# Performance work log

Measured on AMD Instinct MI355X. Metric: run time of the kernel, lower is better.

## Reference

```python
import jax, jax.numpy as jnp
import numpy as np

EPS = 1e-5

def layer_norm(x, g, b):
    mu = jnp.mean(x, axis=-1, keepdims=True)
    var = jnp.mean(jnp.square(x - mu), axis=-1, keepdims=True)
    return (x - mu) * jax.lax.rsqrt(var + EPS) * g + b

def setup_inputs() -> dict:
    key = jax.random.key(0)
    ks = jax.random.split(key, 8)
    B, N, C, H = 1, 384, 128, 128
    s = 0.02
    return {
        "pair": jax.random.normal(ks[0], (B, N, N, C), dtype=jnp.float32),
        "ln_l_g": jnp.ones((C,), jnp.float32), "ln_l_b": jnp.zeros((C,), jnp.float32),
        "ln_r_g": jnp.ones((C,), jnp.float32), "ln_r_b": jnp.zeros((C,), jnp.float32),
        "Wl": jax.random.normal(ks[1], (C, H), jnp.float32) * s, "bl": jnp.zeros((H,), jnp.float32),
        "Wr": jax.random.normal(ks[2], (C, H), jnp.float32) * s, "br": jnp.zeros((H,), jnp.float32),
        "Wg": jax.random.normal(ks[3], (C, H), jnp.float32) * s, "bg": jnp.zeros((H,), jnp.float32),
        "Wo": jax.random.normal(ks[4], (H, C), jnp.float32) * s, "bo": jnp.zeros((C,), jnp.float32),
        "n_g": jnp.ones((C,), jnp.float32), "n_b": jnp.zeros((C,), jnp.float32),
    }

def reference(pair, ln_l_g, ln_l_b, ln_r_g, ln_r_b, Wl, bl, Wr, br, Wg, bg, Wo, bo, n_g, n_b):
    # pair: [B, N, N, C]
    left = layer_norm(pair, ln_l_g, ln_l_b) @ Wl + bl      # [B,N,N,H]
    right = layer_norm(pair, ln_r_g, ln_r_b) @ Wr + br     # [B,N,N,H]
    gate = jax.nn.sigmoid(pair @ Wg + bg)                  # [B,N,N,H]
    # triangle multiplicative update: per-channel N x N matmul over k
    out = jnp.einsum('bikh,bkjh->bijh', left, right)
    out = out * gate
    out = out @ Wo + bo                                    # [B,N,N,C]
    return layer_norm(out + pair, n_g, n_b)
```

## Files before the change

### kernel.cpp

```cpp
#include <hip/hip_runtime.h>
#include <hip/hip_bf16.h>

#define N_ 384
#define C_ 128
#define M_ (N_*N_)

typedef __attribute__((ext_vector_type(8))) short bf16x8_t;
typedef __attribute__((ext_vector_type(4))) float f32x4_t;
typedef unsigned int u32;
typedef unsigned short u16;
typedef unsigned long long u64;

__device__ __forceinline__ u16 f2bf(float f) {
  u32 u = __builtin_bit_cast(u32, f);
  u32 r = (u + 0x7FFFu + ((u >> 16) & 1u)) >> 16;
  return (u16)r;
}
__device__ __forceinline__ float bf2f(u16 h) {
  u32 u = ((u32)h) << 16;
  return __builtin_bit_cast(float, u);
}

__global__ __launch_bounds__(256) void k_prep(const float* __restrict__ lg, const float* __restrict__ rg,
    const float* __restrict__ Wl, const float* __restrict__ Wr, const float* __restrict__ Wg,
    const float* __restrict__ Wo,
    const float* __restrict__ lb, const float* __restrict__ rb,
    const float* __restrict__ bl, const float* __restrict__ br, const float* __restrict__ bg,
    u16* __restrict__ wcat, u16* __restrict__ wot,
    float* __restrict__ bcat, float* __restrict__ sg) {
  int bx = blockIdx.x, t = threadIdx.x;
  if (bx < 256) {
    int idx = bx*256 + t;
    if (idx < 49152) {
      int n = idx >> 7, k = idx & 127;
      float v;
      if (n < 128)      v = lg[k] * Wl[k*128 + n];
      else if (n < 256) v = rg[k] * Wr[k*128 + (n-128)];
      else              v = Wg[k*128 + (n-256)];
      wcat[idx] = f2bf(v);
    } else {
      int i2 = idx - 49152;
      int c = i2 >> 7, h = i2 & 127;
      wot[i2] = f2bf(Wo[h*128 + c]);
    }
  } else if (bx == 256) {
    float s = 0.f;
    if (t < 128)      { for (int k=0;k<128;k++) s += lb[k]*Wl[k*128+t];       s += bl[t];     bcat[t] = s; }
    else              { int hh=t-128; for (int k=0;k<128;k++) s += rb[k]*Wr[k*128+hh]; s += br[hh]; bcat[t] = s; }
  } else {
    if (t < 128)      { bcat[256+t] = bg[t]; }
    else              { int hh = t-128; float s=0.f; for (int k=0;k<128;k++) s += Wg[k*128+hh]; sg[hh] = s; }
  }
}

#define LDK 136
#define LDA 72
#define LDW 72
#define LDT 136

__global__ __launch_bounds__(512) void k_projln(const float* __restrict__ pair,
    const u16* __restrict__ wcat, const float* __restrict__ bcat, const float* __restrict__ sg,
    u16* __restrict__ lr_, u16* __restrict__ gate_) {
  __shared__ u16 At[128*LDK];
  __shared__ float mu_s[128];
  __shared__ float irs_s[128];
  int bx = blockIdx.x;
  int r0 = bx * 128;
  int t = threadIdx.x, w = t>>6, lane = t&63;
  int q = lane>>4, nl = lane&15;

  {
    int rr = t >> 2, quarter = t & 3;
    const float4* gp = (const float4*)(pair + (size_t)(r0+rr)*128 + quarter*32);
    float4 v[8];
    #pragma unroll
    for (int i=0;i<8;i++) v[i] = gp[i];
    float s=0.f, qq=0.f;
    #pragma unroll
    for (int i=0;i<8;i++) {
      s  += v[i].x + v[i].y + v[i].z + v[i].w;
      qq += v[i].x*v[i].x + v[i].y*v[i].y + v[i].z*v[i].z + v[i].w*v[i].w;
    }
    s  += __shfl_xor(s, 1, 64);
    s  += __shfl_xor(s, 2, 64);
    qq += __shfl_xor(qq, 1, 64);
    qq += __shfl_xor(qq, 2, 64);
    float mu = s * (1.f/128.f);
    float var = qq*(1.f/128.f) - mu*mu;
    float rstd = rsqrtf(var + 1e-5f);
    if (quarter == 0) { mu_s[rr] = mu; irs_s[rr] = 1.0f/rstd; }
    u32* lp = (u32*)(At + rr*LDK + quarter*32);
    #pragma unroll
    for (int i=0;i<4;i++) {
      u32 p0 = (u32)f2bf((v[2*i].x-mu)*rstd)   | ((u32)f2bf((v[2*i].y-mu)*rstd)<<16);
      u32 p1 = (u32)f2bf((v[2*i].z-mu)*rstd)   | ((u32)f2bf((v[2*i].w-mu)*rstd)<<16);
      u32 p2 = (u32)f2bf((v[2*i+1].x-mu)*rstd) | ((u32)f2bf((v[2*i+1].y-mu)*rstd)<<16);
      u32 p3 = (u32)f2bf((v[2*i+1].z-mu)*rstd) | ((u32)f2bf((v[2*i+1].w-mu)*rstd)<<16);
      ((uint4*)lp)[i] = make_uint4(p0,p1,p2,p3);
    }
  }
  __syncthreads();

  #pragma unroll 1
  for (int nb = 0; nb < 3; ++nb) {
    const u16* bbase = wcat + (size_t)(nb*128)*128;
    f32x4_t acc[8] = {};
    #pragma unroll
    for (int ks=0; ks<4; ks++) {
      int kel = ks*32 + q*8;
      bf16x8_t b = *(const bf16x8_t*)(bbase + (size_t)(w*16 + nl)*128 + kel);
      #pragma unroll
      for (int tm=0;tm<8;tm++) {
        bf16x8_t a = *(const bf16x8_t*)(At + (tm*16+nl)*LDK + kel);
        acc[tm] = __builtin_amdgcn_mfma_f32_16x16x32_bf16(a, b, acc[tm], 0,0,0);
      }
    }
    int n = w*16 + nl;
    float bias = bcat[nb*128 + n];
    u16* rowp;
    if (nb == 0)      rowp = lr_   + ((size_t)bx*256 + n)*128;
    else if (nb == 1) rowp = lr_   + ((size_t)bx*256 + 128 + n)*128;
    else              rowp = gate_ + ((size_t)bx*128 + n)*128;
    if (nb == 2) {
      float sgn = sg[n];
      #pragma unroll
      for (int tm=0;tm<8;tm++) {
        f32x4_t mu4 = *(const f32x4_t*)(mu_s  + tm*16 + q*4);
        f32x4_t ir4 = *(const f32x4_t*)(irs_s + tm*16 + q*4);
        float v0 = acc[tm][0]*ir4[0] + mu4[0]*sgn + bias;
        float v1 = acc[tm][1]*ir4[1] + mu4[1]*sgn + bias;
        float v2 = acc[tm][2]*ir4[2] + mu4[2]*sgn + bias;
        float v3 = acc[tm][3]*ir4[3] + mu4[3]*sgn + bias;
        v0 = 1.0f/(1.0f+__expf(-v0));
        v1 = 1.0f/(1.0f+__expf(-v1));
        v2 = 1.0f/(1.0f+__expf(-v2));
        v3 = 1.0f/(1.0f+__expf(-v3));
        u32 pk0 = (u32)f2bf(v0) | ((u32)f2bf(v1)<<16);
        u32 pk1 = (u32)f2bf(v2) | ((u32)f2bf(v3)<<16);
        *(u64*)(rowp + tm*16 + q*4) = (u64)pk0 | ((u64)pk1<<32);
      }
    } else {
      #pragma unroll
      for (int tm=0;tm<8;tm++) {
        u32 pk0 = (u32)f2bf(acc[tm][0]+bias) | ((u32)f2bf(acc[tm][1]+bias)<<16);
        u32 pk1 = (u32)f2bf(acc[tm][2]+bias) | ((u32)f2bf(acc[tm][3]+bias)<<16);
        *(u64*)(rowp + tm*16 + q*4) = (u64)pk0 | ((u64)pk1<<32);
      }
    }
  }
}

__global__ __launch_bounds__(512) void k_einsum(const u16* __restrict__ lr_,
    const u16* __restrict__ gate_, u16* __restrict__ og_) {
  __shared__ u16 smem[2*128*LDA];
  u16* At = smem; u16* Bt = smem + 128*LDA;
  int bx = blockIdx.x;
  int wk = (bx & 7) * 144 + (bx >> 3);
  int h = wk / 9; int rem = wk % 9;
  int i0 = (rem/3)*128, j0c = rem%3;
  int t = threadIdx.x, w = t>>6, lane = t&63;
  int q = lane>>4, nl = lane&15;
  f32x4_t acc[4][2] = {};
  int m0 = (w&1)*64, nb0 = (w>>1)*32;
  for (int kb = 0; kb < N_; kb += 64) {
    int c = kb >> 7, off = kb & 127;
    {
      int rr = t>>2, quarter = t&3;
      const u16* gp = lr_ + (((size_t)(i0+rr)*3 + c)*256 + h)*128 + off + quarter*16;
      u16* lp = At + rr*LDA + quarter*16;
      ((uint4*)lp)[0] = ((const uint4*)gp)[0];
      ((uint4*)lp)[1] = ((const uint4*)gp)[1];
    }
    {
      int kk2 = t>>4;
      int seg = t&15;
      const u16* g0 = lr_ + (((size_t)(kb + 2*kk2)*3 + j0c)*256 + 128 + h)*128 + seg*8;
      const u16* g1 = g0 + 3*256*128;
      uint4 ra = ((const uint4*)g0)[0];
      uint4 rbv = ((const uint4*)g1)[0];
      u32 w0[4] = {ra.x,ra.y,ra.z,ra.w};
      u32 w1[4] = {rbv.x,rbv.y,rbv.z,rbv.w};
      u32 sw = (u32)(seg>>1) << 4;
      char* bbytes = (char*)Bt;
      #pragma unroll
      for (int e=0;e<4;e++) {
        u32 lo = w0[e], hi = w1[e];
        u32 evenw = (lo & 0xffffu) | (hi << 16);
        u32 oddw  = (lo >> 16)     | (hi & 0xffff0000u);
        int je = seg*8 + 2*e;
        u32 byteE = ((u32)(je*LDA + 2*kk2) * 2u) ^ sw;
        u32 byteO = ((u32)((je+1)*LDA + 2*kk2) * 2u) ^ sw;
        *(u32*)(bbytes + byteE) = evenw;
        *(u32*)(bbytes + byteO) = oddw;
      }
    }
    __syncthreads();
    #pragma unroll
    for (int ks=0; ks<2; ks++) {
      int kel = ks*32 + q*8;
      bf16x8_t a[4], b[2];
      #pragma unroll
      for (int tm=0;tm<4;tm++) a[tm] = *(const bf16x8_t*)(At + (m0+tm*16+nl)*LDA + kel);
      #pragma unroll
      for (int tn=0;tn<2;tn++) {
        u32 swr = (u32)(((nb0>>4) + tn) & 7) << 4;
        b[tn] = *(const bf16x8_t*)((const char*)Bt + ((u32)(((nb0+tn*16+nl)*LDA + kel)*2) ^ swr));
      }
      #pragma unroll
      for (int tm=0;tm<4;tm++)
        #pragma unroll
        for (int tn=0;tn<2;tn++)
          acc[tm][tn] = __builtin_amdgcn_mfma_f32_16x16x32_bf16(a[tm], b[tn], acc[tm][tn], 0,0,0);
    }
    __syncthreads();
  }
  u16* Ot = smem;
  #pragma unroll
  for (int tm=0;tm<4;tm++)
    #pragma unroll
    for (int tn=0;tn<2;tn++)
      #pragma unroll
      for (int p=0;p<4;p++) {
        int m = m0 + tm*16 + q*4 + p;
        int n = nb0 + tn*16 + nl;
        Ot[m*LDT + n] = f2bf(acc[tm][tn][p]);
      }
  __syncthreads();
  {
    int m = t>>2, hq = t&3;
    size_t gbase = (((size_t)(i0+m)*3 + j0c)*128 + h)*128 + hq*32;
    const uint4* gg = (const uint4*)(gate_ + gbase);
    const uint4* lo = (const uint4*)(Ot + m*LDT + hq*32);
    uint4* od = (uint4*)(og_ + gbase);
    #pragma unroll
    for (int i=0;i<4;i++) {
      uint4 gv = gg[i]; uint4 ov = lo[i];
      u32 ga[4] = {gv.x,gv.y,gv.z,gv.w};
      u32 oa[4] = {ov.x,ov.y,ov.z,ov.w};
      u32 ra2[4];
      #pragma unroll
      for (int e=0;e<4;e++) {
        float g0 = bf2f((u16)(ga[e]&0xffffu)), g1 = bf2f((u16)(ga[e]>>16));
        float o0 = bf2f((u16)(oa[e]&0xffffu)), o1 = bf2f((u16)(oa[e]>>16));
        ra2[e] = (u32)f2bf(o0*g0) | ((u32)f2bf(o1*g1)<<16);
      }
      od[i] = make_uint4(ra2[0],ra2[1],ra2[2],ra2[3]);
    }
  }
}

__global__ __launch_bounds__(512) void k_final(const u16* __restrict__ og_, const u16* __restrict__ wot,
    const float* __restrict__ pair, const float* __restrict__ bo,
    const float* __restrict__ ng, const float* __restrict__ nb_,
    float* __restrict__ out) {
  __shared__ u16 smem[2*128*LDW];
  u16* At = smem; u16* Wt = smem + 128*LDW;
  int bx = blockIdx.x;
  int r0 = bx * 128;
  int t = threadIdx.x, w = t>>6, lane = t&63;
  int q = lane>>4, nl = lane&15;
  f32x4_t acc[8] = {};
  int m0 = w*16;
  for (int c0 = 0; c0 < 128; c0 += 64) {
    {
      int hh = t>>3, seg = t&7;
      const u16* gp = og_ + ((size_t)bx*128 + (c0+hh))*128 + seg*16;
      uint4 b0 = ((const uint4*)gp)[0];
      uint4 b1 = ((const uint4*)gp)[1];
      u32 xs[8] = {b0.x,b0.y,b0.z,b0.w,b1.x,b1.y,b1.z,b1.w};
      #pragma unroll
      for (int e=0;e<8;e++) {
        int rb = seg*16 + 2*e;
        At[(rb+0)*LDW+hh] = (u16)(xs[e]&0xffffu);
        At[(rb+1)*LDW+hh] = (u16)(xs[e]>>16);
      }
    }
    {
      int c = t>>2, q4 = t&3;
      const u16* gp = wot + (size_t)c*128 + c0 + q4*16;
      u16* lp = Wt + c*LDW + q4*16;
      ((uint4*)lp)[0] = ((const uint4*)gp)[0];
      ((uint4*)lp)[1] = ((const uint4*)gp)[1];
    }
    __syncthreads();
    #pragma unroll
    for (int ks=0; ks<2; ks++) {
      int kel = ks*32 + q*8;
      bf16x8_t a = *(const bf16x8_t*)(At + (m0+nl)*LDW + kel);
      bf16x8_t b[8];
      #pragma unroll
      for (int tn=0;tn<8;tn++) b[tn] = *(const bf16x8_t*)(Wt + (tn*16+nl)*LDW + kel);
      #pragma unroll
      for (int tn=0;tn<8;tn++)
        acc[tn] = __builtin_amdgcn_mfma_f32_16x16x32_bf16(a, b[tn], acc[tn], 0,0,0);
    }
    __syncthreads();
  }
  float rsum[4], rsq[4];
  #pragma unroll
  for (int p=0;p<4;p++) { rsum[p]=0.f; rsq[p]=0.f; }
  #pragma unroll
  for (int tn=0;tn<8;tn++) {
    int n = tn*16 + nl;
    float bb = bo[n];
    #pragma unroll
    for (int p=0;p<4;p++) {
      int m = m0 + q*4 + p;
      float v = acc[tn][p] + bb + pair[(size_t)(r0+m)*128 + n];
      acc[tn][p] = v;
      rsum[p] += v;
      rsq[p]  += v*v;
    }
  }
  #pragma unroll
  for (int msk=1; msk<16; msk<<=1) {
    #pragma unroll
    for (int p=0;p<4;p++) {
      rsum[p] += __shfl_xor(rsum[p], msk, 64);
      rsq[p]  += __shfl_xor(rsq[p],  msk, 64);
    }
  }
  #pragma unroll
  for (int p=0;p<4;p++) {
    float mu = rsum[p] * (1.f/128.f);
    float var = rsq[p]*(1.f/128.f) - mu*mu;
    rsum[p] = mu;
    rsq[p] = rsqrtf(var + 1e-5f);
  }
  #pragma unroll
  for (int tn=0;tn<8;tn++) {
    int n = tn*16 + nl;
    float g = ng[n], b2 = nb_[n];
    #pragma unroll
    for (int p=0;p<4;p++) {
      int m = m0 + q*4 + p;
      out[(size_t)(r0+m)*128 + n] = (acc[tn][p] - rsum[p]) * rsq[p] * g + b2;
    }
  }
}

extern "C" void kernel_launch(void* const* d_in, const int* in_sizes, int n_in,
                              void* d_out, int out_size, void* d_ws, size_t ws_size,
                              hipStream_t stream) {
  (void)in_sizes; (void)n_in; (void)out_size; (void)ws_size;
  const float* pair   = (const float*)d_in[0];
  const float* ln_l_g = (const float*)d_in[1];
  const float* ln_l_b = (const float*)d_in[2];
  const float* ln_r_g = (const float*)d_in[3];
  const float* ln_r_b = (const float*)d_in[4];
  const float* Wl = (const float*)d_in[5];
  const float* bl = (const float*)d_in[6];
  const float* Wr = (const float*)d_in[7];
  const float* br = (const float*)d_in[8];
  const float* Wg = (const float*)d_in[9];
  const float* bg = (const float*)d_in[10];
  const float* Wo = (const float*)d_in[11];
  const float* bo = (const float*)d_in[12];
  const float* n_g = (const float*)d_in[13];
  const float* n_b = (const float*)d_in[14];

  char* ws = (char*)d_ws;
  const size_t SZ = (size_t)M_*128*sizeof(u16);
  u16*  og    = (u16*)(ws);
  u16*  gate  = (u16*)(ws + SZ);
  u16*  wcat  = (u16*)(ws + 2*SZ);
  float* bcat = (float*)(ws + 2*SZ + 98304);
  float* sgp  = (float*)(ws + 2*SZ + 98304 + 1536);
  u16*  wot   = (u16*)(ws + 2*SZ + 98304 + 1536 + 512);

  u16* lr = (u16*)d_out;

  k_prep<<<258, 256, 0, stream>>>(ln_l_g, ln_r_g, Wl, Wr, Wg, Wo,
                                  ln_l_b, ln_r_b, bl, br, bg, wcat, wot, bcat, sgp);
  k_projln<<<1152, 512, 0, stream>>>(pair, wcat, bcat, sgp, lr, gate);
  k_einsum<<<1152, 512, 0, stream>>>(lr, gate, og);
  k_final<<<1152, 512, 0, stream>>>(og, wot, pair, bo, n_g, n_b, (float*)d_out);
}
```

Measured before the change: 268.9 us.

## Register-prefetch next tiles in einsum and final kernels, swizzle final A transpose

The einsum kernel now loads the next k-block's A and B tiles into registers while the current block is being computed, so global loads overlap the MFMA work. The final kernel loads the full Wo tile once up front into a wider LDS buffer and register-prefetches the second half of the og tile. It also replaces the scalar 16-bit transposing LDS stores with paired 32-bit swizzled stores, matching the einsum B path. The cost is higher register pressure and more LDS in the final kernel, which may reduce occupancy.

```diff
diff --git a/kernel.cpp b/kernel.cpp
--- a/kernel.cpp
+++ b/kernel.cpp
@@ -56,6 +56,7 @@
 #define LDK 136
 #define LDA 72
 #define LDW 72
+#define LDW2 136
 #define LDT 136
 
 __global__ __launch_bounds__(512) void k_projln(const float* __restrict__ pair,
@@ -162,24 +163,27 @@
   int q = lane>>4, nl = lane&15;
   f32x4_t acc[4][2] = {};
   int m0 = (w&1)*64, nb0 = (w>>1)*32;
-  for (int kb = 0; kb < N_; kb += 64) {
-    int c = kb >> 7, off = kb & 127;
+
+  int rrA = t>>2, quarterA = t&3;
+  int kk2 = t>>4, seg = t&15;
+
+  uint4 aR0, aR1, bR0, bR1;
+  {
+    const u16* ga = lr_ + (((size_t)(i0+rrA)*3 + 0)*256 + h)*128 + quarterA*16;
+    aR0 = ((const uint4*)ga)[0]; aR1 = ((const uint4*)ga)[1];
+    const u16* g0 = lr_ + (((size_t)(2*kk2)*3 + j0c)*256 + 128 + h)*128 + seg*8;
+    bR0 = ((const uint4*)g0)[0];
+    bR1 = ((const uint4*)(g0 + 3*256*128))[0];
+  }
+  #pragma unroll 1
+  for (int s = 0; s < 6; ++s) {
     {
-      int rr = t>>2, quarter = t&3;
-      const u16* gp = lr_ + (((size_t)(i0+rr)*3 + c)*256 + h)*128 + off + quarter*16;
-      u16* lp = At + rr*LDA + quarter*16;
-      ((uint4*)lp)[0] = ((const uint4*)gp)[0];
-      ((uint4*)lp)[1] = ((const uint4*)gp)[1];
+      u16* lp = At + rrA*LDA + quarterA*16;
+      ((uint4*)lp)[0] = aR0; ((uint4*)lp)[1] = aR1;
     }
     {
-      int kk2 = t>>4;
-      int seg = t&15;
-      const u16* g0 = lr_ + (((size_t)(kb + 2*kk2)*3 + j0c)*256 + 128 + h)*128 + seg*8;
-      const u16* g1 = g0 + 3*256*128;
-      uint4 ra = ((const uint4*)g0)[0];
-      uint4 rbv = ((const uint4*)g1)[0];
-      u32 w0[4] = {ra.x,ra.y,ra.z,ra.w};
-      u32 w1[4] = {rbv.x,rbv.y,rbv.z,rbv.w};
+      u32 w0[4] = {bR0.x,bR0.y,bR0.z,bR0.w};
+      u32 w1[4] = {bR1.x,bR1.y,bR1.z,bR1.w};
       u32 sw = (u32)(seg>>1) << 4;
       char* bbytes = (char*)Bt;
       #pragma unroll
@@ -188,11 +192,17 @@
         u32 evenw = (lo & 0xffffu) | (hi << 16);
         u32 oddw  = (lo >> 16)     | (hi & 0xffff0000u);
         int je = seg*8 + 2*e;
-        u32 byteE = ((u32)(je*LDA + 2*kk2) * 2u) ^ sw;
-        u32 byteO = ((u32)((je+1)*LDA + 2*kk2) * 2u) ^ sw;
-        *(u32*)(bbytes + byteE) = evenw;
-        *(u32*)(bbytes + byteO) = oddw;
-      }
+        *(u32*)(bbytes + (((u32)(je*LDA + 2*kk2) * 2u) ^ sw)) = evenw;
+        *(u32*)(bbytes + (((u32)((je+1)*LDA + 2*kk2) * 2u) ^ sw)) = oddw;
+      }
+    }
+    if (s < 5) {
+      int kb = (s+1)*64; int c = kb>>7, off = kb&127;
+      const u16* ga = lr_ + (((size_t)(i0+rrA)*3 + c)*256 + h)*128 + off + quarterA*16;
+      aR0 = ((const uint4*)ga)[0]; aR1 = ((const uint4*)ga)[1];
+      const u16* g0 = lr_ + (((size_t)(kb + 2*kk2)*3 + j0c)*256 + 128 + h)*128 + seg*8;
+      bR0 = ((const uint4*)g0)[0];
+      bR1 = ((const uint4*)(g0 + 3*256*128))[0];
     }
     __syncthreads();
     #pragma unroll
@@ -253,43 +263,61 @@
     const float* __restrict__ pair, const float* __restrict__ bo,
     const float* __restrict__ ng, const float* __restrict__ nb_,
     float* __restrict__ out) {
-  __shared__ u16 smem[2*128*LDW];
-  u16* At = smem; u16* Wt = smem + 128*LDW;
+  __shared__ u16 At[128*LDW];
+  __shared__ u16 Wt[128*LDW2];
   int bx = blockIdx.x;
   int r0 = bx * 128;
   int t = threadIdx.x, w = t>>6, lane = t&63;
   int q = lane>>4, nl = lane&15;
   f32x4_t acc[8] = {};
   int m0 = w*16;
-  for (int c0 = 0; c0 < 128; c0 += 64) {
+  int hh2 = t>>4, seg = t&15;
+
+  uint4 aR0, aR1;
+  {
+    const u16* g0 = og_ + ((size_t)bx*128 + 2*hh2)*128 + seg*8;
+    aR0 = ((const uint4*)g0)[0];
+    aR1 = ((const uint4*)(g0 + 128))[0];
+  }
+  {
+    int c = t>>2, q4 = t&3;
+    const u16* gp = wot + (size_t)c*128 + q4*32;
+    u16* lp = Wt + c*LDW2 + q4*32;
+    #pragma unroll
+    for (int i=0;i<4;i++) ((uint4*)lp)[i] = ((const uint4*)gp)[i];
+  }
+  #pragma unroll
+  for (int step=0; step<2; ++step) {
     {
-      int hh = t>>3, seg = t&7;
-      const u16* gp = og_ + ((size_t)bx*128 + (c0+hh))*128 + seg*16;
-      uint4 b0 = ((const uint4*)gp)[0];
-      uint4 b1 = ((const uint4*)gp)[1];
-      u32 xs[8] = {b0.x,b0.y,b0.z,b0.w,b1.x,b1.y,b1.z,b1.w};
-      #pragma unroll
-      for (int e=0;e<8;e++) {
-        int rb = seg*16 + 2*e;
-        At[(rb+0)*LDW+hh] = (u16)(xs[e]&0xffffu);
-        At[(rb+1)*LDW+hh] = (u16)(xs[e]>>16);
-      }
-    }
-    {
-      int c = t>>2, q4 = t&3;
-      const u16* gp = wot + (size_t)c*128 + c0 + q4*16;
-      u16* lp = Wt + c*LDW + q4*16;
-      ((uint4*)lp)[0] = ((const uint4*)gp)[0];
-      ((uint4*)lp)[1] = ((const uint4*)gp)[1];
+      u32 w0[4] = {aR0.x,aR0.y,aR0.z,aR0.w};
+      u32 w1[4] = {aR1.x,aR1.y,aR1.z,aR1.w};
+      u32 sw = (u32)(seg>>1) << 4;
+      char* abytes = (char*)At;
+      #pragma unroll
+      for (int e=0;e<4;e++) {
+        u32 lo = w0[e], hi = w1[e];
+        u32 evenw = (lo & 0xffffu) | (hi << 16);
+        u32 oddw  = (lo >> 16)     | (hi & 0xffff0000u);
+        int je = seg*8 + 2*e;
+        *(u32*)(abytes + (((u32)(je*LDW + 2*hh2) * 2u) ^ sw)) = evenw;
+        *(u32*)(abytes + (((u32)((je+1)*LDW + 2*hh2) * 2u) ^ sw)) = oddw;
+      }
+    }
+    if (step == 0) {
+      const u16* g0 = og_ + ((size_t)bx*128 + 64 + 2*hh2)*128 + seg*8;
+      aR0 = ((const uint4*)g0)[0];
+      aR1 = ((const uint4*)(g0 + 128))[0];
     }
     __syncthreads();
+    int c0 = step*64;
     #pragma unroll
     for (int ks=0; ks<2; ks++) {
       int kel = ks*32 + q*8;
-      bf16x8_t a = *(const bf16x8_t*)(At + (m0+nl)*LDW + kel);
+      bf16x8_t a = *(const bf16x8_t*)((const char*)At +
+                     ((u32)(((m0+nl)*LDW + kel)*2) ^ ((u32)w << 4)));
       bf16x8_t b[8];
       #pragma unroll
-      for (int tn=0;tn<8;tn++) b[tn] = *(const bf16x8_t*)(Wt + (tn*16+nl)*LDW + kel);
+      for (int tn=0;tn<8;tn++) b[tn] = *(const bf16x8_t*)(Wt + (tn*16+nl)*LDW2 + c0 + kel);
       #pragma unroll
       for (int tn=0;tn<8;tn++)
         acc[tn] = __builtin_amdgcn_mfma_f32_16x16x32_bf16(a, b[tn], acc[tn], 0,0,0);
```

Result: faster. 263.4 us (-2.0%).
